# Kernel tuning notes

Hardware: AMD Instinct MI355X
Metric: run time of the kernel (lower is better)

Reference implementation:

```python
import jax, jax.numpy as jnp
import numpy as np

HE, WE, L = 361, 720, 37   # ERA5 source grid (0.5 deg) and pressure levels
HM, WM, K = 180, 360, 32   # model grid (1 deg) and model sigma levels
EPS = 1e-8

# ERA5 standard 37 pressure levels in Pa (ascending)
P_LEVELS = [100., 200., 300., 500., 700., 1000., 2000., 3000., 5000., 7000.,
            10000., 12500., 15000., 17500., 20000., 22500., 25000., 30000.,
            35000., 40000., 45000., 50000., 55000., 60000., 65000., 70000.,
            75000., 77500., 80000., 82500., 85000., 87500., 90000., 92500.,
            95000., 97500., 100000.]


def setup_inputs() -> dict:
    key = jax.random.key(0)
    ks = jax.random.split(key, 6)
    u = 10.0 * jax.random.normal(ks[0], (HE, WE, L), jnp.float32)
    v = 10.0 * jax.random.normal(ks[1], (HE, WE, L), jnp.float32)
    w = 0.1 * jax.random.normal(ks[2], (HE, WE, L), jnp.float32)
    T = 250.0 + 30.0 * jax.random.normal(ks[3], (HE, WE, L), jnp.float32)
    q = 0.01 * jax.random.uniform(ks[4], (HE, WE, L), jnp.float32)
    ps = 95000.0 + 5000.0 * jax.random.normal(ks[5], (HE, WE), jnp.float32)
    era5_lat = jnp.linspace(-90.0, 90.0, HE, dtype=jnp.float32)
    era5_lon = jnp.linspace(0.0, 359.5, WE, dtype=jnp.float32)
    model_lat = jnp.linspace(-89.0, 89.0, HM, dtype=jnp.float32)
    model_lon = jnp.linspace(0.25, 359.75, WM, dtype=jnp.float32)
    p_levels = jnp.asarray(P_LEVELS, jnp.float32)
    b_k = ((jnp.arange(K, dtype=jnp.float32) + 0.5) / K)
    a_k = 100.0 * (1.0 - b_k)  # simple hybrid coefficients (Pa)
    return dict(u=u, v=v, w=w, T=T, q=q, ps=ps,
                era5_lat=era5_lat, era5_lon=era5_lon,
                model_lat=model_lat, model_lon=model_lon,
                p_levels=p_levels, a_k=a_k, b_k=b_k)


def _axis_interp(grid, pts):
    """1D linear interp indices/weights with linear extrapolation (fill_value=None)."""
    i = jnp.clip(jnp.searchsorted(grid, pts, side='right') - 1, 0, grid.shape[0] - 2)
    t = (pts - grid[i]) / (grid[i + 1] - grid[i])
    return i, t


def _forward(u, v, w, T, q, ps, era5_lat, era5_lon, model_lat, model_lon,
             p_levels, a_k, b_k):
    # ---- horizontal bilinear interp (RegularGridInterpolator, linear) ----
    stacked = jnp.concatenate([u, v, w, T, q, ps[..., None]], axis=-1)  # [HE,WE,5L+1]
    iy, ty = _axis_interp(era5_lat, model_lat)   # [HM]
    ix, tx = _axis_interp(era5_lon, model_lon)   # [WM]
    r0 = stacked[iy]       # [HM,WE,C]
    r1 = stacked[iy + 1]
    d00, d01 = r0[:, ix], r0[:, ix + 1]          # [HM,WM,C]
    d10, d11 = r1[:, ix], r1[:, ix + 1]
    wy = ty[:, None, None]
    wx = tx[None, :, None]
    hd = (1 - wy) * ((1 - wx) * d00 + wx * d01) + wy * ((1 - wx) * d10 + wx * d11)
    vars_h = hd[..., :5 * L].reshape(HM, WM, 5, L)  # [HM,WM,5,L]
    ps_m = hd[..., -1]                               # [HM,WM]

    # ---- model pressure: p = a_k + b_k * ps ----
    p_model = a_k + b_k * ps_m[..., None]            # [HM,WM,K]

    # ---- vertical log-pressure linear interp with per-pixel valid mask ----
    logp_e = jnp.log(p_levels + EPS)                 # [L]
    logp_m = jnp.log(p_model + EPS)                  # [HM,WM,K]
    nvalid = jnp.searchsorted(p_levels, ps_m, side='right')  # levels with p<=ps
    idx = jnp.searchsorted(logp_e, logp_m, side='right') - 1
    idx = jnp.clip(idx, 0, jnp.maximum(nvalid[..., None] - 2, 0))  # [HM,WM,K]
    x0, x1 = logp_e[idx], logp_e[idx + 1]
    t = (logp_m - x0) / (x1 - x0)                    # linear extrapolation at edges
    g0 = jnp.take_along_axis(vars_h, idx[:, :, None, :], axis=3)        # [HM,WM,5,K]
    g1 = jnp.take_along_axis(vars_h, (idx + 1)[:, :, None, :], axis=3)
    out = g0 + t[:, :, None, :] * (g1 - g0)
    out = jnp.where(nvalid[:, :, None, None] >= 2, out, 0.0)            # <2 valid -> 0

    # ---- unit conversion / clamps ----
    u_o, v_o, w_o = out[:, :, 0], out[:, :, 1], out[:, :, 2]
    T_o = jnp.clip(out[:, :, 3], 150.0, 350.0)
    q_o = jnp.clip(out[:, :, 4], 0.0, 0.05)
    ps_o = jnp.clip(ps_m, 30000.0, 110000.0)
    out3d = jnp.stack([u_o, v_o, w_o, T_o, q_o], axis=-1)  # [HM,WM,K,5]
    return out3d, p_model, ps_o


def reference(u, v, w, T, q, ps, era5_lat, era5_lon, model_lat, model_lon,
              p_levels, a_k, b_k):
    return _forward(u, v, w, T, q, ps, era5_lat, era5_lon,
                    model_lat, model_lon, p_levels, a_k, b_k)
```

## Files before the change

### kernel.cpp

```cpp
#include <hip/hip_runtime.h>
#include <cmath>

#define HE 361
#define WE 720
#define LL 37
#define HM 180
#define WM 360
#define KK 32
#define NPTS (HM * WM)
#define EPSF 1e-8f
#define PTSB 8

#define OFF1 ((size_t)HM * WM * KK * 5)
#define OFF2 (OFF1 + (size_t)HM * WM * KK)

#define WS_IY    0
#define WS_TY    180
#define WS_IX    360
#define WS_TX    720
#define WS_LOGPE 1080

__device__ __forceinline__ int upper_bound_g(const float* a, int n, float v) {
    int lo = 0, hi = n;
    while (lo < hi) {
        int m = (lo + hi) >> 1;
        if (a[m] <= v) lo = m + 1; else hi = m;
    }
    return lo;
}

__global__ void precompute_kernel(const float* __restrict__ era5_lat,
                                  const float* __restrict__ era5_lon,
                                  const float* __restrict__ model_lat,
                                  const float* __restrict__ model_lon,
                                  const float* __restrict__ p_levels,
                                  int* __restrict__ ws_iy, float* __restrict__ ws_ty,
                                  int* __restrict__ ws_ix, float* __restrict__ ws_tx,
                                  float* __restrict__ ws_logpe) {
    int t = blockIdx.x * blockDim.x + threadIdx.x;
    if (t < HM) {
        float v = model_lat[t];
        int i = upper_bound_g(era5_lat, HE, v) - 1;
        if (i < 0) i = 0;
        if (i > HE - 2) i = HE - 2;
        ws_iy[t] = i;
        ws_ty[t] = (v - era5_lat[i]) / (era5_lat[i + 1] - era5_lat[i]);
    } else if (t < HM + WM) {
        int j = t - HM;
        float v = model_lon[j];
        int i = upper_bound_g(era5_lon, WE, v) - 1;
        if (i < 0) i = 0;
        if (i > WE - 2) i = WE - 2;
        ws_ix[j] = i;
        ws_tx[j] = (v - era5_lon[i]) / (era5_lon[i + 1] - era5_lon[i]);
    } else if (t < HM + WM + LL) {
        int k = t - HM - WM;
        ws_logpe[k] = logf(p_levels[k] + EPSF);
    }
}

__global__ void __launch_bounds__(256)
fused_kernel(const float* __restrict__ u, const float* __restrict__ v,
             const float* __restrict__ w, const float* __restrict__ T,
             const float* __restrict__ q, const float* __restrict__ ps,
             const float* __restrict__ p_levels,
             const float* __restrict__ a_k, const float* __restrict__ b_k,
             const int* __restrict__ ws_iy, const float* __restrict__ ws_ty,
             const int* __restrict__ ws_ix, const float* __restrict__ ws_tx,
             const float* __restrict__ ws_logpe,
             float* __restrict__ out) {
    __shared__ float s_h[PTSB][5 * LL];
    __shared__ float s_psm[PTSB];
    __shared__ int   s_maxi[PTSB];
    __shared__ int   s_inval[PTSB];
    __shared__ float s_logpe[LL];
    __shared__ float s_ak[KK];
    __shared__ float s_bk[KK];

    const int tid = threadIdx.x;
    if (tid < LL) {
        s_logpe[tid] = ws_logpe[tid];
    } else if (tid >= 64 && tid < 64 + KK) {
        s_ak[tid - 64] = a_k[tid - 64];
        s_bk[tid - 64] = b_k[tid - 64];
    }

    const int pt_local = tid >> 5;
    const int grp      = tid & 31;
    const int pt = blockIdx.x * PTSB + pt_local;
    const int y  = pt / WM;
    const int x  = pt - y * WM;

    const int   iy = ws_iy[y];
    const float ty = ws_ty[y];
    const int   ix = ws_ix[x];
    const float tx = ws_tx[x];
    const float omty = 1.0f - ty;
    const float omtx = 1.0f - tx;

    const size_t b00 = (size_t)iy * WE + ix;

    if (grp == 0) {
        const float p00 = ps[b00], p01 = ps[b00 + 1];
        const float p10 = ps[b00 + WE], p11 = ps[b00 + WE + 1];
        const float ps_m = omty * (omtx * p00 + tx * p01) + ty * (omtx * p10 + tx * p11);
        s_psm[pt_local] = ps_m;
        const int nvalid = upper_bound_g(p_levels, LL, ps_m);
        int maxi = nvalid - 2;
        if (maxi < 0) maxi = 0;
        s_maxi[pt_local]  = maxi;
        s_inval[pt_local] = (nvalid < 2) ? 1 : 0;
        out[OFF2 + pt] = fminf(fmaxf(ps_m, 30000.0f), 110000.0f);
    }

    const float* srcs0 = u;
    const float* srcs1 = v;
    const float* srcs2 = w;
    const float* srcs3 = T;
    const float* srcs4 = q;

#pragma unroll
    for (int it = 0; it < 6; it++) {
        const int ch = grp + 32 * it;
        if (ch < 5 * LL) {
            const int var = ch / LL;
            const int l   = ch - var * LL;
            const float* s = (var == 0) ? srcs0 : (var == 1) ? srcs1
                           : (var == 2) ? srcs2 : (var == 3) ? srcs3 : srcs4;
            const size_t c00 = b00 * LL + l;
            const float d00 = s[c00];
            const float d01 = s[c00 + LL];
            const float d10 = s[c00 + (size_t)WE * LL];
            const float d11 = s[c00 + (size_t)WE * LL + LL];
            s_h[pt_local][ch] = omty * (omtx * d00 + tx * d01) +
                                ty   * (omtx * d10 + tx * d11);
        }
    }

    __syncthreads();

    const int k = grp;
    const float ps_m = s_psm[pt_local];
    const int   maxi = s_maxi[pt_local];
    const bool  invalid = (s_inval[pt_local] != 0);

    const float pm = s_ak[k] + s_bk[k] * ps_m;
    out[OFF1 + (size_t)pt * KK + k] = pm;

    const float lpm = logf(pm + EPSF);
    int lo = 0, hi = LL;
    while (lo < hi) {
        int m = (lo + hi) >> 1;
        if (s_logpe[m] <= lpm) lo = m + 1; else hi = m;
    }
    int i = lo - 1;
    if (i < 0) i = 0;
    if (i > maxi) i = maxi;
    const float t = (lpm - s_logpe[i]) / (s_logpe[i + 1] - s_logpe[i]);

    const size_t obase = (size_t)pt * (KK * 5) + k * 5;
#pragma unroll
    for (int var = 0; var < 5; var++) {
        const float g0 = s_h[pt_local][var * LL + i];
        const float g1 = s_h[pt_local][var * LL + i + 1];
        float o = g0 + t * (g1 - g0);
        if (invalid) o = 0.0f;
        if (var == 3) o = fminf(fmaxf(o, 150.0f), 350.0f);
        if (var == 4) o = fminf(fmaxf(o, 0.0f), 0.05f);
        out[obase + var] = o;
    }
}

extern "C" void kernel_launch(void* const* d_in, const int* in_sizes, int n_in,
                              void* d_out, int out_size, void* d_ws, size_t ws_size,
                              hipStream_t stream) {
    const float* u         = (const float*)d_in[0];
    const float* v         = (const float*)d_in[1];
    const float* w         = (const float*)d_in[2];
    const float* T         = (const float*)d_in[3];
    const float* q         = (const float*)d_in[4];
    const float* ps        = (const float*)d_in[5];
    const float* era5_lat  = (const float*)d_in[6];
    const float* era5_lon  = (const float*)d_in[7];
    const float* model_lat = (const float*)d_in[8];
    const float* model_lon = (const float*)d_in[9];
    const float* p_levels  = (const float*)d_in[10];
    const float* a_k       = (const float*)d_in[11];
    const float* b_k       = (const float*)d_in[12];

    float* wsf = (float*)d_ws;
    int*   ws_iy    = (int*)(wsf + WS_IY);
    float* ws_ty    = wsf + WS_TY;
    int*   ws_ix    = (int*)(wsf + WS_IX);
    float* ws_tx    = wsf + WS_TX;
    float* ws_logpe = wsf + WS_LOGPE;

    float* out = (float*)d_out;

    precompute_kernel<<<3, 256, 0, stream>>>(era5_lat, era5_lon, model_lat, model_lon,
                                             p_levels, ws_iy, ws_ty, ws_ix, ws_tx,
                                             ws_logpe);

    const int blocks = NPTS / PTSB;
    fused_kernel<<<blocks, 256, 0, stream>>>(u, v, w, T, q, ps, p_levels, a_k, b_k,
                                             ws_iy, ws_ty, ws_ix, ws_tx, ws_logpe, out);
}
```

Measured before the change: 236.4 us.

## Make fused kernel wave-local, hoist all loads, and stage output through LDS

Each 64-lane wavefront now handles its two points on its own. It uses a per-wave copy of the log-pressure table and drops the block-wide __syncthreads. All five variables' bilinear corner loads (plus the tail levels 32-36) are issued up front into registers to expose memory-level parallelism, and indexing switches to 32-bit. The vertically interpolated outputs are staged in LDS and written back with fully coalesced 64-wide stores instead of stride-5 per-thread stores. Correctness now depends on lockstep wave execution and compiler ordering of LDS accesses, since there is no explicit barrier between the s_h writes and reads.

Measured after the change: 232.9 us. Within noise of the previous version (-1.5%).

```diff
diff --git a/kernel.cpp b/kernel.cpp
--- a/kernel.cpp
+++ b/kernel.cpp
@@ -10,6 +10,7 @@
 #define NPTS (HM * WM)
 #define EPSF 1e-8f
 #define PTSB 8
+#define WE37 (WE * LL)
 
 #define OFF1 ((size_t)HM * WM * KK * 5)
 #define OFF2 (OFF1 + (size_t)HM * WM * KK)
@@ -73,23 +74,21 @@
     __shared__ float s_psm[PTSB];
     __shared__ int   s_maxi[PTSB];
     __shared__ int   s_inval[PTSB];
-    __shared__ float s_logpe[LL];
-    __shared__ float s_ak[KK];
-    __shared__ float s_bk[KK];
-
-    const int tid = threadIdx.x;
-    if (tid < LL) {
-        s_logpe[tid] = ws_logpe[tid];
-    } else if (tid >= 64 && tid < 64 + KK) {
-        s_ak[tid - 64] = a_k[tid - 64];
-        s_bk[tid - 64] = b_k[tid - 64];
-    }
-
+    __shared__ float s_logpe[4][LL];
+    __shared__ float s_out[4][2 * KK * 5];
+
+    const int tid      = threadIdx.x;
+    const int wv       = tid >> 6;
+    const int lane     = tid & 63;
     const int pt_local = tid >> 5;
     const int grp      = tid & 31;
+
+    if (lane < LL) s_logpe[wv][lane] = ws_logpe[lane];
+
+    const int y  = (blockIdx.x * PTSB) / WM;
+    const int x0 = blockIdx.x * PTSB - y * WM;
+    const int x  = x0 + pt_local;
     const int pt = blockIdx.x * PTSB + pt_local;
-    const int y  = pt / WM;
-    const int x  = pt - y * WM;
 
     const int   iy = ws_iy[y];
     const float ty = ws_ty[y];
@@ -98,7 +97,31 @@
     const float omty = 1.0f - ty;
     const float omtx = 1.0f - tx;
 
-    const size_t b00 = (size_t)iy * WE + ix;
+    const int b00  = iy * WE + ix;
+    const int base = b00 * LL;
+    const int i0   = base + grp;
+    const int i1   = base + grp + WE37;
+
+    float a00[5], a01[5], a10[5], a11[5];
+#define LD4(slot, S) \
+    a00[slot] = S[i0];      a01[slot] = S[i0 + LL]; \
+    a10[slot] = S[i1];      a11[slot] = S[i1 + LL];
+    LD4(0, u) LD4(1, v) LD4(2, w) LD4(3, T) LD4(4, q)
+#undef LD4
+
+    const bool tval = (grp < 25);
+    int tvar = grp / 5;
+    int tl   = 32 + (grp - tvar * 5);
+    if (!tval) { tvar = 0; tl = 32; }
+    const float* ts = (tvar == 0) ? u : (tvar == 1) ? v
+                    : (tvar == 2) ? w : (tvar == 3) ? T : q;
+    const int ti0 = base + tl;
+    const int ti1 = base + tl + WE37;
+    const float t00 = ts[ti0], t01 = ts[ti0 + LL];
+    const float t10 = ts[ti1], t11 = ts[ti1 + LL];
+
+    const float ak = a_k[grp];
+    const float bk = b_k[grp];
 
     if (grp == 0) {
         const float p00 = ps[b00], p01 = ps[b00 + 1];
@@ -113,52 +136,38 @@
         out[OFF2 + pt] = fminf(fmaxf(ps_m, 30000.0f), 110000.0f);
     }
 
-    const float* srcs0 = u;
-    const float* srcs1 = v;
-    const float* srcs2 = w;
-    const float* srcs3 = T;
-    const float* srcs4 = q;
-
 #pragma unroll
-    for (int it = 0; it < 6; it++) {
-        const int ch = grp + 32 * it;
-        if (ch < 5 * LL) {
-            const int var = ch / LL;
-            const int l   = ch - var * LL;
-            const float* s = (var == 0) ? srcs0 : (var == 1) ? srcs1
-                           : (var == 2) ? srcs2 : (var == 3) ? srcs3 : srcs4;
-            const size_t c00 = b00 * LL + l;
-            const float d00 = s[c00];
-            const float d01 = s[c00 + LL];
-            const float d10 = s[c00 + (size_t)WE * LL];
-            const float d11 = s[c00 + (size_t)WE * LL + LL];
-            s_h[pt_local][ch] = omty * (omtx * d00 + tx * d01) +
-                                ty   * (omtx * d10 + tx * d11);
-        }
-    }
-
-    __syncthreads();
-
-    const int k = grp;
-    const float ps_m = s_psm[pt_local];
-    const int   maxi = s_maxi[pt_local];
+    for (int it = 0; it < 5; it++) {
+        const float hv = omty * (omtx * a00[it] + tx * a01[it]) +
+                         ty   * (omtx * a10[it] + tx * a11[it]);
+        s_h[pt_local][it * LL + grp] = hv;
+    }
+    {
+        const float hv = omty * (omtx * t00 + tx * t01) + ty * (omtx * t10 + tx * t11);
+        if (tval) s_h[pt_local][tvar * LL + tl] = hv;
+    }
+
+    const int   k       = grp;
+    const float ps_m    = s_psm[pt_local];
+    const int   maxi    = s_maxi[pt_local];
     const bool  invalid = (s_inval[pt_local] != 0);
 
-    const float pm = s_ak[k] + s_bk[k] * ps_m;
+    const float pm = ak + bk * ps_m;
     out[OFF1 + (size_t)pt * KK + k] = pm;
 
     const float lpm = logf(pm + EPSF);
     int lo = 0, hi = LL;
     while (lo < hi) {
         int m = (lo + hi) >> 1;
-        if (s_logpe[m] <= lpm) lo = m + 1; else hi = m;
+        if (s_logpe[wv][m] <= lpm) lo = m + 1; else hi = m;
     }
     int i = lo - 1;
     if (i < 0) i = 0;
     if (i > maxi) i = maxi;
-    const float t = (lpm - s_logpe[i]) / (s_logpe[i + 1] - s_logpe[i]);
-
-    const size_t obase = (size_t)pt * (KK * 5) + k * 5;
+    const float t = (lpm - s_logpe[wv][i]) / (s_logpe[wv][i + 1] - s_logpe[wv][i]);
+
+    const int half = lane >> 5;
+    float* so = &s_out[wv][half * (KK * 5)];
 #pragma unroll
     for (int var = 0; var < 5; var++) {
         const float g0 = s_h[pt_local][var * LL + i];
@@ -167,7 +176,15 @@
         if (invalid) o = 0.0f;
         if (var == 3) o = fminf(fmaxf(o, 150.0f), 350.0f);
         if (var == 4) o = fminf(fmaxf(o, 0.0f), 0.05f);
-        out[obase + var] = o;
+        so[k * 5 + var] = o;
+    }
+
+    __builtin_amdgcn_wave_barrier();
+
+    const size_t ob = (size_t)(blockIdx.x * PTSB + 2 * wv) * (KK * 5);
+#pragma unroll
+    for (int c = 0; c < 5; c++) {
+        out[ob + lane + 64 * c] = s_out[wv][lane + 64 * c];
     }
 }
 
```
